# Kernel tuning notes

Hardware: AMD Instinct MI355X
Metric: run time of the kernel (lower is better)

Reference implementation:

```python
import math
import jax, jax.numpy as jnp
import numpy as np

D_MODEL, STATE_DIM, SEQ_L = 256, 64, 8192


def setup_inputs() -> dict:
    key = jax.random.key(0)
    ks = jax.random.split(key, 6)
    d, N = D_MODEL, STATE_DIM
    s = 1.0 / math.sqrt(N)
    return {
        "Lambda_re": jax.random.normal(ks[0], (d, N), jnp.float32),
        "Lambda_im": jax.random.normal(ks[1], (d, N), jnp.float32),
        "P_re": jax.random.normal(ks[2], (d, N), jnp.float32) * s,
        "P_im": jax.random.normal(ks[3], (d, N), jnp.float32) * s,
        "B_re": jax.random.normal(ks[4], (d, N), jnp.float32) * s,
        "B_im": jnp.zeros((d, N), jnp.float32),
        "log_dt": jax.random.uniform(ks[5], (d,), jnp.float32,
                                     math.log(1e-3), math.log(0.1)),
        "D": jnp.zeros((d,), jnpp := jnp.float32) if False else jnp.zeros((d,), jnp.float32),
        "L": SEQ_L,
    }


def reference(Lambda_re, Lambda_im, P_re, P_im, B_re, B_im, log_dt, D, L):
    # NPLR / Cauchy-Woodbury S4 kernel (learn_cd=False -> C = B, D is a zero buffer)
    Lam = (-jax.nn.softplus(Lambda_re) + 1j * Lambda_im).astype(jnp.complex64)  # [d, N]
    P = (P_re + 1j * P_im).astype(jnp.complex64)                                # [d, N]
    B = (B_re + 1j * B_im).astype(jnp.complex64)                                # [d, N]
    dt = jnp.exp(log_dt)                                                        # [d]

    k = jnp.arange(L)
    z = jnp.exp((-2j * jnp.pi / L) * k).astype(jnp.complex64)                   # [L] roots of unity
    eps = jnp.finfo(jnp.float32).eps
    denom_z = 1.0 + z
    denom_z = jnp.where(jnp.abs(denom_z) < eps, jnp.complex64(eps), denom_z)

    # Bilinear-transform frequencies g: [d, L] complex
    g = (2.0 / dt)[:, None] * ((1.0 - z) / denom_z)[None, :]

    # Cauchy resolvent R: [d, L, N] complex (the dominant intermediate)
    R = 1.0 / (g[:, :, None] - Lam[:, None, :])

    Pc, Bc = jnp.conj(P), jnp.conj(B)
    PRB = jnp.einsum('dn,dln,dn->dl', Pc, R, B)
    PRP = jnp.einsum('dn,dln,dn->dl', Pc, R, P)
    BRB = jnp.einsum('dn,dln,dn->dl', Bc, R, B)
    BRP = jnp.einsum('dn,dln,dn->dl', Bc, R, P)

    # Woodbury rank-1 correction, then undo the bilinear prefactor
    K_hat = (2.0 / denom_z)[None, :] * (BRB - BRP * PRB / (1.0 + PRP))          # [d, L]
    K = jnp.fft.ifft(K_hat, n=L, axis=-1).real.astype(jnp.float32)
    return (K, D)
```

## Files before the change

### kernel.cpp

```cpp
#include <hip/hip_runtime.h>
#include <math.h>

#ifndef M_PI
#define M_PI 3.14159265358979323846
#endif

#define DMODEL 256
#define NSTATE 64
#define LSEQ   8192
#define INVL   (1.0f/8192.0f)

#define OFF_TW  0
#define OFF_DN  (6144*8)
#define OFF_CDT (OFF_DN + DMODEL*NSTATE*48)

__device__ __forceinline__ float sin_rev(float r) {
#if __has_builtin(__builtin_amdgcn_sinf)
  return __builtin_amdgcn_sinf(r);
#else
  return __sinf(r * 6.283185307179586f);
#endif
}
__device__ __forceinline__ float cos_rev(float r) {
#if __has_builtin(__builtin_amdgcn_cosf)
  return __builtin_amdgcn_cosf(r);
#else
  return __cosf(r * 6.283185307179586f);
#endif
}

__device__ __forceinline__ float2 cmul(float2 a, float2 b) {
  return make_float2(a.x*b.x - a.y*b.y, a.x*b.y + a.y*b.x);
}

__device__ __forceinline__ float2 woodbury(float2 S1, float2 S2, float2 S3,
                                           float2 S4, float T) {
  float nr = (S1.x*S1.x - S1.y*S1.y) + (S2.x*S2.x - S2.y*S2.y);
  float ni = 2.0f*(S1.x*S1.y + S2.x*S2.y);
  float dr = 1.0f + S3.x, di = S3.y;
  float inv = __builtin_amdgcn_rcpf(fmaf(dr, dr, di*di));
  float qr = (nr*dr + ni*di) * inv;
  float qi = (ni*dr - nr*di) * inv;
  float vr = S4.x - qr, vi = S4.y - qi;
  return make_float2((vr - T*vi)*INVL, (vi + T*vr)*INVL);
}

__global__ __launch_bounds__(256) void precompute_kernel(
    const float* __restrict__ Lre, const float* __restrict__ Lim,
    const float* __restrict__ Pre, const float* __restrict__ Pim,
    const float* __restrict__ Bre, const float* __restrict__ Bim,
    const float* __restrict__ log_dt, char* __restrict__ ws)
{
  const int t = blockIdx.x * blockDim.x + threadIdx.x;
  float2* tw  = (float2*)(ws + OFF_TW);
  float4* dn  = (float4*)(ws + OFF_DN);
  float*  cdt = (float*)(ws + OFF_CDT);

  if (t < 6144) {
    double th = (2.0 * M_PI / (double)LSEQ) * (double)t;
    double s, c; sincos(th, &s, &c);
    tw[t] = make_float2((float)c, (float)s);
  }
  {
    float lre = Lre[t], lim = Lim[t];
    float pre = Pre[t], pim = Pim[t];
    float bre = Bre[t], bim = Bim[t];
    float sp = fmaxf(lre, 0.0f) + log1pf(expf(-fabsf(lre)));
    float w1r = pre*bre + pim*bim;
    float w1i = pre*bim - pim*bre;
    float w2  = pre*pre + pim*pim;
    float w3  = bre*bre + bim*bim;
    dn[3*t]   = make_float4(lim, sp*sp, w1r, w1i);
    dn[3*t+1] = make_float4(w2, w3, w1r*sp, w1i*sp);
    dn[3*t+2] = make_float4(w2*sp, w3*sp, 0.0f, 0.0f);
  }
  if (t < DMODEL) cdt[t] = 2.0f * expf(-log_dt[t]);
}

__global__ __launch_bounds__(1024) void fused_kernel(
    const float4* __restrict__ dn_all, const float* __restrict__ cdt,
    const float2* __restrict__ tw, const float* __restrict__ Din,
    float* __restrict__ out)
{
  __shared__ __align__(16) float2 xy[LSEQ];
  const int d = blockIdx.x;
  const int t = threadIdx.x;
  const float4* dn = dn_all + (size_t)d * (3*NSTATE);
  const float c = cdt[d];

  float TA[4], TB[4], gA[4], gB[4];
  float2 S[4][8];
#pragma unroll
  for (int j = 0; j < 4; ++j) {
    const int b = t + (j << 10);
    const unsigned p = (unsigned)(2*b);
    const unsigned r = __brev(p) >> 19;
    const int kA = (int)((r & 0x1000u) | ((r & 0x0555u) << 1) | ((r & 0x0AAAu) >> 1));
    const float rev = (float)kA * (1.0f/16384.0f);
    const float sA = sin_rev(rev), cA = cos_rev(rev);
    float ta = sA * __builtin_amdgcn_rcpf(cA);
    float tb = -cA * __builtin_amdgcn_rcpf(sA);
    ta = fminf(fmaxf(ta, -1e7f), 1e7f);
    tb = fminf(fmaxf(tb, -1e7f), 1e7f);
    TA[j] = ta; TB[j] = tb;
    gA[j] = c * ta; gB[j] = c * tb;
#pragma unroll
    for (int q = 0; q < 8; ++q) S[j][q] = make_float2(0.0f, 0.0f);
  }

#pragma unroll 4
  for (int n = 0; n < NSTATE; ++n) {
    const float4 q0 = dn[3*n];
    const float4 q1 = dn[3*n+1];
    const float4 q2 = dn[3*n+2];
#pragma unroll
    for (int j = 0; j < 4; ++j) {
      {
        const float dim = gA[j] - q0.x;
        const float inv = __builtin_amdgcn_rcpf(fmaf(dim, dim, q0.y));
        const float v = dim * inv;
        S[j][0].x = fmaf(q1.z, inv, S[j][0].x);  S[j][0].y = fmaf(-q0.z, v, S[j][0].y);
        S[j][1].x = fmaf(q1.w, inv, S[j][1].x);  S[j][1].y = fmaf(-q0.w, v, S[j][1].y);
        S[j][2].x = fmaf(q2.x, inv, S[j][2].x);  S[j][2].y = fmaf(-q1.x, v, S[j][2].y);
        S[j][3].x = fmaf(q2.y, inv, S[j][3].x);  S[j][3].y = fmaf(-q1.y, v, S[j][3].y);
      }
      {
        const float dim = gB[j] - q0.x;
        const float inv = __builtin_amdgcn_rcpf(fmaf(dim, dim, q0.y));
        const float v = dim * inv;
        S[j][4].x = fmaf(q1.z, inv, S[j][4].x);  S[j][4].y = fmaf(-q0.z, v, S[j][4].y);
        S[j][5].x = fmaf(q1.w, inv, S[j][5].x);  S[j][5].y = fmaf(-q0.w, v, S[j][5].y);
        S[j][6].x = fmaf(q2.x, inv, S[j][6].x);  S[j][6].y = fmaf(-q1.x, v, S[j][6].y);
        S[j][7].x = fmaf(q2.y, inv, S[j][7].x);  S[j][7].y = fmaf(-q1.y, v, S[j][7].y);
      }
    }
  }

#pragma unroll
  for (int j = 0; j < 4; ++j) {
    const float2 KA = woodbury(S[j][0], S[j][1], S[j][2], S[j][3], TA[j]);
    const float2 KB = woodbury(S[j][4], S[j][5], S[j][6], S[j][7], TB[j]);
    ((float4*)xy)[t + (j << 10)] = make_float4(KA.x + KB.x, KA.y + KB.y,
                                               KA.x - KB.x, KA.y - KB.y);
  }
  __syncthreads();

#pragma unroll
  for (int s = 0; s < 6; ++s) {
    const int h = 2 << (2*s);
    const int twsh = 10 - 2*s;
#pragma unroll
    for (int j = 0; j < 2; ++j) {
      const int bb = t + (j << 10);
      const int pos = bb & (h - 1);
      const int i0 = ((bb >> (1 + 2*s)) << (3 + 2*s)) + pos;
      const int ti = pos << twsh;
      const float2 w1 = tw[ti];
      const float2 w2 = tw[2*ti];
      const float2 w3 = tw[3*ti];
      const float2 x0 = xy[i0];
      const float2 x1 = xy[i0 + h];
      const float2 x2 = xy[i0 + 2*h];
      const float2 x3 = xy[i0 + 3*h];
      const float2 t1 = cmul(w1, x1);
      const float2 t2 = cmul(w2, x2);
      const float2 t3 = cmul(w3, x3);
      const float2 u0 = make_float2(x0.x + t2.x, x0.y + t2.y);
      const float2 u1 = make_float2(x0.x - t2.x, x0.y - t2.y);
      const float2 u2 = make_float2(t1.x + t3.x, t1.y + t3.y);
      const float2 vv = make_float2(t1.x - t3.x, t1.y - t3.y);
      xy[i0]         = make_float2(u0.x + u2.x, u0.y + u2.y);
      xy[i0 + h]     = make_float2(u1.x - vv.y, u1.y + vv.x);
      xy[i0 + 2*h]   = make_float2(u0.x - u2.x, u0.y - u2.y);
      xy[i0 + 3*h]   = make_float2(u1.x + vv.y, u1.y - vv.x);
    }
    __syncthreads();
  }

  float* orow = out + (size_t)d * LSEQ;
#pragma unroll
  for (int j = 0; j < 8; ++j) orow[t + (j << 10)] = xy[t + (j << 10)].x;

  if (d == 0 && t < DMODEL) out[(size_t)DMODEL * LSEQ + t] = Din[t];
}

extern "C" void kernel_launch(void* const* d_in, const int* in_sizes, int n_in,
                              void* d_out, int out_size, void* d_ws, size_t ws_size,
                              hipStream_t stream)
{
  const float* Lre    = (const float*)d_in[0];
  const float* Lim    = (const float*)d_in[1];
  const float* Pre    = (const float*)d_in[2];
  const float* Pim    = (const float*)d_in[3];
  const float* Bre    = (const float*)d_in[4];
  const float* Bim    = (const float*)d_in[5];
  const float* log_dt = (const float*)d_in[6];
  const float* Din    = (const float*)d_in[7];
  float* out = (float*)d_out;
  char* ws = (char*)d_ws;

  hipLaunchKernelGGL(precompute_kernel, dim3(64), dim3(256), 0, stream,
                     Lre, Lim, Pre, Pim, Bre, Bim, log_dt, ws);
  hipLaunchKernelGGL(fused_kernel, dim3(DMODEL), dim3(1024), 0, stream,
                     (const float4*)(ws + OFF_DN), (const float*)(ws + OFF_CDT),
                     (const float2*)(ws + OFF_TW), Din, out);
}
```

Baseline: 124.9 us.

## Vectorize Cauchy accumulation with packed FP32 ops and split into two passes

Rewrites the per-state Cauchy inner loop to use v_pk_add/mul/fma_f32 on A/B frequency pairs, with a duplicated, pre-negated parameter layout (five float4 per state) so packed operands line up. The four frequency groups per thread are processed in two passes of two to cut live accumulator registers, and launch bounds now request a minimum occupancy. This halves VALU instruction count in the hot loop but adds more global/cache loads per state and a serial outer loop.

```diff
diff --git a/kernel.cpp b/kernel.cpp
--- a/kernel.cpp
+++ b/kernel.cpp
@@ -12,7 +12,7 @@
 
 #define OFF_TW  0
 #define OFF_DN  (6144*8)
-#define OFF_CDT (OFF_DN + DMODEL*NSTATE*48)
+#define OFF_CDT (OFF_DN + DMODEL*NSTATE*80)
 
 __device__ __forceinline__ float sin_rev(float r) {
 #if __has_builtin(__builtin_amdgcn_sinf)
@@ -31,6 +31,16 @@
 
 __device__ __forceinline__ float2 cmul(float2 a, float2 b) {
   return make_float2(a.x*b.x - a.y*b.y, a.x*b.y + a.y*b.x);
+}
+
+__device__ __forceinline__ float2 pk_add(float2 a, float2 b) {
+  float2 d; asm("v_pk_add_f32 %0, %1, %2" : "=v"(d) : "v"(a), "v"(b)); return d;
+}
+__device__ __forceinline__ float2 pk_mul(float2 a, float2 b) {
+  float2 d; asm("v_pk_mul_f32 %0, %1, %2" : "=v"(d) : "v"(a), "v"(b)); return d;
+}
+__device__ __forceinline__ float2 pk_fma(float2 a, float2 b, float2 c) {
+  float2 d; asm("v_pk_fma_f32 %0, %1, %2, %3" : "=v"(d) : "v"(a), "v"(b), "v"(c)); return d;
 }
 
 __device__ __forceinline__ float2 woodbury(float2 S1, float2 S2, float2 S3,
@@ -70,14 +80,16 @@
     float w1i = pre*bim - pim*bre;
     float w2  = pre*pre + pim*pim;
     float w3  = bre*bre + bim*bim;
-    dn[3*t]   = make_float4(lim, sp*sp, w1r, w1i);
-    dn[3*t+1] = make_float4(w2, w3, w1r*sp, w1i*sp);
-    dn[3*t+2] = make_float4(w2*sp, w3*sp, 0.0f, 0.0f);
+    dn[5*t]   = make_float4(-lim, -lim, sp*sp, sp*sp);
+    dn[5*t+1] = make_float4(w1r*sp, w1r*sp, w1i*sp, w1i*sp);
+    dn[5*t+2] = make_float4(w2*sp, w2*sp, w3*sp, w3*sp);
+    dn[5*t+3] = make_float4(-w1r, -w1r, -w1i, -w1i);
+    dn[5*t+4] = make_float4(-w2, -w2, -w3, -w3);
   }
   if (t < DMODEL) cdt[t] = 2.0f * expf(-log_dt[t]);
 }
 
-__global__ __launch_bounds__(1024) void fused_kernel(
+__global__ __launch_bounds__(1024, 4) void fused_kernel(
     const float4* __restrict__ dn_all, const float* __restrict__ cdt,
     const float2* __restrict__ tw, const float* __restrict__ Din,
     float* __restrict__ out)
@@ -85,63 +97,84 @@
   __shared__ __align__(16) float2 xy[LSEQ];
   const int d = blockIdx.x;
   const int t = threadIdx.x;
-  const float4* dn = dn_all + (size_t)d * (3*NSTATE);
   const float c = cdt[d];
 
-  float TA[4], TB[4], gA[4], gB[4];
-  float2 S[4][8];
-#pragma unroll
-  for (int j = 0; j < 4; ++j) {
-    const int b = t + (j << 10);
-    const unsigned p = (unsigned)(2*b);
-    const unsigned r = __brev(p) >> 19;
-    const int kA = (int)((r & 0x1000u) | ((r & 0x0555u) << 1) | ((r & 0x0AAAu) >> 1));
-    const float rev = (float)kA * (1.0f/16384.0f);
-    const float sA = sin_rev(rev), cA = cos_rev(rev);
-    float ta = sA * __builtin_amdgcn_rcpf(cA);
-    float tb = -cA * __builtin_amdgcn_rcpf(sA);
-    ta = fminf(fmaxf(ta, -1e7f), 1e7f);
-    tb = fminf(fmaxf(tb, -1e7f), 1e7f);
-    TA[j] = ta; TB[j] = tb;
-    gA[j] = c * ta; gB[j] = c * tb;
-#pragma unroll
-    for (int q = 0; q < 8; ++q) S[j][q] = make_float2(0.0f, 0.0f);
-  }
-
-#pragma unroll 4
-  for (int n = 0; n < NSTATE; ++n) {
-    const float4 q0 = dn[3*n];
-    const float4 q1 = dn[3*n+1];
-    const float4 q2 = dn[3*n+2];
-#pragma unroll
-    for (int j = 0; j < 4; ++j) {
-      {
-        const float dim = gA[j] - q0.x;
-        const float inv = __builtin_amdgcn_rcpf(fmaf(dim, dim, q0.y));
-        const float v = dim * inv;
-        S[j][0].x = fmaf(q1.z, inv, S[j][0].x);  S[j][0].y = fmaf(-q0.z, v, S[j][0].y);
-        S[j][1].x = fmaf(q1.w, inv, S[j][1].x);  S[j][1].y = fmaf(-q0.w, v, S[j][1].y);
-        S[j][2].x = fmaf(q2.x, inv, S[j][2].x);  S[j][2].y = fmaf(-q1.x, v, S[j][2].y);
-        S[j][3].x = fmaf(q2.y, inv, S[j][3].x);  S[j][3].y = fmaf(-q1.y, v, S[j][3].y);
+  const float4* dnv = dn_all + (size_t)d * (5*NSTATE);
+  asm("" : "+v"(dnv));
+
+  for (int pass = 0; pass < 2; ++pass) {
+    float TA[2], TB[2];
+    float2 gAB[2];
+    float2 S[2][8];
+#pragma unroll
+    for (int j = 0; j < 2; ++j) {
+      const int b = t + ((2*pass + j) << 10);
+      const unsigned p = (unsigned)(2*b);
+      const unsigned r = __brev(p) >> 19;
+      const int kA = (int)((r & 0x1000u) | ((r & 0x0555u) << 1) | ((r & 0x0AAAu) >> 1));
+      const float rev = (float)kA * (1.0f/16384.0f);
+      const float sA = sin_rev(rev), cA = cos_rev(rev);
+      float ta = sA * __builtin_amdgcn_rcpf(cA);
+      float tb = -cA * __builtin_amdgcn_rcpf(sA);
+      ta = fminf(fmaxf(ta, -1e7f), 1e7f);
+      tb = fminf(fmaxf(tb, -1e7f), 1e7f);
+      TA[j] = ta; TB[j] = tb;
+      gAB[j] = make_float2(c * ta, c * tb);
+#pragma unroll
+      for (int q = 0; q < 8; ++q) S[j][q] = make_float2(0.0f, 0.0f);
+    }
+
+#pragma unroll 2
+    for (int n = 0; n < NSTATE; ++n) {
+      const float4 e0 = dnv[5*n];
+      const float4 e1 = dnv[5*n+1];
+      const float4 e2 = dnv[5*n+2];
+      const float4 e3 = dnv[5*n+3];
+      const float4 e4 = dnv[5*n+4];
+      const float2 nl2  = make_float2(e0.x, e0.y);
+      const float2 s2_2 = make_float2(e0.z, e0.w);
+      const float2 w1rs = make_float2(e1.x, e1.y);
+      const float2 w1is = make_float2(e1.z, e1.w);
+      const float2 w2s  = make_float2(e2.x, e2.y);
+      const float2 w3s  = make_float2(e2.z, e2.w);
+      const float2 nw1r = make_float2(e3.x, e3.y);
+      const float2 nw1i = make_float2(e3.z, e3.w);
+      const float2 nw2  = make_float2(e4.x, e4.y);
+      const float2 nw3  = make_float2(e4.z, e4.w);
+#pragma unroll
+      for (int j = 0; j < 2; ++j) {
+        const float2 dimAB = pk_add(gAB[j], nl2);
+        const float2 denAB = pk_fma(dimAB, dimAB, s2_2);
+        float2 invAB;
+        invAB.x = __builtin_amdgcn_rcpf(denAB.x);
+        invAB.y = __builtin_amdgcn_rcpf(denAB.y);
+        const float2 vAB = pk_mul(dimAB, invAB);
+        S[j][0] = pk_fma(w1rs, invAB, S[j][0]);
+        S[j][1] = pk_fma(w1is, invAB, S[j][1]);
+        S[j][2] = pk_fma(w2s,  invAB, S[j][2]);
+        S[j][3] = pk_fma(w3s,  invAB, S[j][3]);
+        S[j][4] = pk_fma(nw1r, vAB, S[j][4]);
+        S[j][5] = pk_fma(nw1i, vAB, S[j][5]);
+        S[j][6] = pk_fma(nw2,  vAB, S[j][6]);
+        S[j][7] = pk_fma(nw3,  vAB, S[j][7]);
       }
-      {
-        const float dim = gB[j] - q0.x;
-        const float inv = __builtin_amdgcn_rcpf(fmaf(dim, dim, q0.y));
-        const float v = dim * inv;
-        S[j][4].x = fmaf(q1.z, inv, S[j][4].x);  S[j][4].y = fmaf(-q0.z, v, S[j][4].y);
-        S[j][5].x = fmaf(q1.w, inv, S[j][5].x);  S[j][5].y = fmaf(-q0.w, v, S[j][5].y);
-        S[j][6].x = fmaf(q2.x, inv, S[j][6].x);  S[j][6].y = fmaf(-q1.x, v, S[j][6].y);
-        S[j][7].x = fmaf(q2.y, inv, S[j][7].x);  S[j][7].y = fmaf(-q1.y, v, S[j][7].y);
-      }
-    }
-  }
-
-#pragma unroll
-  for (int j = 0; j < 4; ++j) {
-    const float2 KA = woodbury(S[j][0], S[j][1], S[j][2], S[j][3], TA[j]);
-    const float2 KB = woodbury(S[j][4], S[j][5], S[j][6], S[j][7], TB[j]);
-    ((float4*)xy)[t + (j << 10)] = make_float4(KA.x + KB.x, KA.y + KB.y,
-                                               KA.x - KB.x, KA.y - KB.y);
+    }
+
+#pragma unroll
+    for (int j = 0; j < 2; ++j) {
+      const float2 S1A = make_float2(S[j][0].x, S[j][4].x);
+      const float2 S2A = make_float2(S[j][1].x, S[j][5].x);
+      const float2 S3A = make_float2(S[j][2].x, S[j][6].x);
+      const float2 S4A = make_float2(S[j][3].x, S[j][7].x);
+      const float2 S1B = make_float2(S[j][0].y, S[j][4].y);
+      const float2 S2B = make_float2(S[j][1].y, S[j][5].y);
+      const float2 S3B = make_float2(S[j][2].y, S[j][6].y);
+      const float2 S4B = make_float2(S[j][3].y, S[j][7].y);
+      const float2 KA = woodbury(S1A, S2A, S3A, S4A, TA[j]);
+      const float2 KB = woodbury(S1B, S2B, S3B, S4B, TB[j]);
+      ((float4*)xy)[t + ((2*pass + j) << 10)] =
+          make_float4(KA.x + KB.x, KA.y + KB.y, KA.x - KB.x, KA.y - KB.y);
+    }
   }
   __syncthreads();
 
```

Measured after the change: 161.6 us. +29.4%, slower.

## Split Cauchy+FFT per channel into four segment blocks plus global final radix-4 pass

Applied to the files above, without the earlier changes.

The Cauchy evaluation and the first FFT stages move into a kernel that launches four 512-thread blocks per channel, each owning a 2048-point segment in shared memory. The last radix-4 stage runs in a separate finish kernel that reads the segments from a global workspace. This replaces 256 large 1024-thread blocks with 1024 smaller ones to raise occupancy and CU coverage, and the Cauchy inner loop now keeps one frequency pair per thread, cutting register pressure. The cost is a global round trip of the full complex spectrum and an extra launch. The fused kernel is kept as a fallback when the workspace is too small.

```diff
diff --git a/kernel.cpp b/kernel.cpp
--- a/kernel.cpp
+++ b/kernel.cpp
@@ -13,6 +13,8 @@
 #define OFF_TW  0
 #define OFF_DN  (6144*8)
 #define OFF_CDT (OFF_DN + DMODEL*NSTATE*48)
+#define OFF_XY  (OFF_CDT + 1024)
+#define WS_NEED ((size_t)OFF_XY + (size_t)DMODEL*LSEQ*8)
 
 __device__ __forceinline__ float sin_rev(float r) {
 #if __has_builtin(__builtin_amdgcn_sinf)
@@ -45,6 +47,65 @@
   return make_float2((vr - T*vi)*INVL, (vi + T*vr)*INVL);
 }
 
+__device__ __forceinline__ void radix4(float2& x0, float2& x1, float2& x2, float2& x3,
+                                       float2 w1, float2 w2, float2 w3) {
+  const float2 t1 = cmul(w1, x1);
+  const float2 t2 = cmul(w2, x2);
+  const float2 t3 = cmul(w3, x3);
+  const float2 u0 = make_float2(x0.x + t2.x, x0.y + t2.y);
+  const float2 u1 = make_float2(x0.x - t2.x, x0.y - t2.y);
+  const float2 u2 = make_float2(t1.x + t3.x, t1.y + t3.y);
+  const float2 vv = make_float2(t1.x - t3.x, t1.y - t3.y);
+  x0 = make_float2(u0.x + u2.x, u0.y + u2.y);
+  x1 = make_float2(u1.x - vv.y, u1.y + vv.x);
+  x2 = make_float2(u0.x - u2.x, u0.y - u2.y);
+  x3 = make_float2(u1.x + vv.y, u1.y - vv.x);
+}
+
+__device__ __forceinline__ float4 cauchy_pair(const float4* __restrict__ dnp,
+                                              const float c, const int b) {
+  const unsigned p = (unsigned)(2*b);
+  const unsigned r = __brev(p) >> 19;
+  const int kA = (int)((r & 0x1000u) | ((r & 0x0555u) << 1) | ((r & 0x0AAAu) >> 1));
+  const float rev = (float)kA * (1.0f/16384.0f);
+  const float sA = sin_rev(rev), cA = cos_rev(rev);
+  float TA = sA * __builtin_amdgcn_rcpf(cA);
+  float TB = -cA * __builtin_amdgcn_rcpf(sA);
+  TA = fminf(fmaxf(TA, -1e7f), 1e7f);
+  TB = fminf(fmaxf(TB, -1e7f), 1e7f);
+  const float gA = c * TA, gB = c * TB;
+
+  float2 s1a={0,0}, s2a={0,0}, s3a={0,0}, s4a={0,0};
+  float2 s1b={0,0}, s2b={0,0}, s3b={0,0}, s4b={0,0};
+#pragma unroll 2
+  for (int n = 0; n < NSTATE; ++n) {
+    const float4 q0 = dnp[3*n];
+    const float4 q1 = dnp[3*n+1];
+    const float4 q2 = dnp[3*n+2];
+    {
+      const float dim = q0.x - gA;
+      const float inv = __builtin_amdgcn_rcpf(fmaf(dim, dim, q0.y));
+      const float v = dim * inv;
+      s1a.x = fmaf(q0.z, inv, s1a.x);  s1a.y = fmaf(q1.z, v, s1a.y);
+      s2a.x = fmaf(q0.w, inv, s2a.x);  s2a.y = fmaf(q1.w, v, s2a.y);
+      s3a.x = fmaf(q1.x, inv, s3a.x);  s3a.y = fmaf(q2.x, v, s3a.y);
+      s4a.x = fmaf(q1.y, inv, s4a.x);  s4a.y = fmaf(q2.y, v, s4a.y);
+    }
+    {
+      const float dim = q0.x - gB;
+      const float inv = __builtin_amdgcn_rcpf(fmaf(dim, dim, q0.y));
+      const float v = dim * inv;
+      s1b.x = fmaf(q0.z, inv, s1b.x);  s1b.y = fmaf(q1.z, v, s1b.y);
+      s2b.x = fmaf(q0.w, inv, s2b.x);  s2b.y = fmaf(q1.w, v, s2b.y);
+      s3b.x = fmaf(q1.x, inv, s3b.x);  s3b.y = fmaf(q2.x, v, s3b.y);
+      s4b.x = fmaf(q1.y, inv, s4b.x);  s4b.y = fmaf(q2.y, v, s4b.y);
+    }
+  }
+  const float2 KA = woodbury(s1a, s2a, s3a, s4a, TA);
+  const float2 KB = woodbury(s1b, s2b, s3b, s4b, TB);
+  return make_float4(KA.x + KB.x, KA.y + KB.y, KA.x - KB.x, KA.y - KB.y);
+}
+
 __global__ __launch_bounds__(256) void precompute_kernel(
     const float* __restrict__ Lre, const float* __restrict__ Lim,
     const float* __restrict__ Pre, const float* __restrict__ Pim,
@@ -70,11 +131,78 @@
     float w1i = pre*bim - pim*bre;
     float w2  = pre*pre + pim*pim;
     float w3  = bre*bre + bim*bim;
-    dn[3*t]   = make_float4(lim, sp*sp, w1r, w1i);
-    dn[3*t+1] = make_float4(w2, w3, w1r*sp, w1i*sp);
-    dn[3*t+2] = make_float4(w2*sp, w3*sp, 0.0f, 0.0f);
+    dn[3*t]   = make_float4(lim, sp*sp, w1r*sp, w1i*sp);
+    dn[3*t+1] = make_float4(w2*sp, w3*sp, w1r, w1i);
+    dn[3*t+2] = make_float4(w2, w3, 0.0f, 0.0f);
   }
   if (t < DMODEL) cdt[t] = 2.0f * expf(-log_dt[t]);
+}
+
+__global__ __launch_bounds__(512, 8) void cauchyfft_kernel(
+    const float4* __restrict__ dn_all, const float* __restrict__ cdt,
+    const float2* __restrict__ tw, float2* __restrict__ xy_ws)
+{
+  __shared__ __align__(16) float2 xy[2048];
+  const int d   = blockIdx.x >> 2;
+  const int seg = blockIdx.x & 3;
+  const int t   = threadIdx.x;
+  const float c = cdt[d];
+  const float4* dnp = dn_all + (size_t)d * (3*NSTATE);
+
+#pragma unroll
+  for (int pass = 0; pass < 2; ++pass) {
+    const int bl = t + (pass << 9);
+    ((float4*)xy)[bl] = cauchy_pair(dnp, c, (seg << 10) + bl);
+  }
+  __syncthreads();
+
+#pragma unroll
+  for (int s = 0; s < 4; ++s) {
+    const int h = 2 << (2*s);
+    const int twsh = 10 - 2*s;
+    const int pos = t & (h - 1);
+    const int i0 = ((t >> (1 + 2*s)) << (3 + 2*s)) + pos;
+    const int ti = pos << twsh;
+    float2 x0 = xy[i0], x1 = xy[i0 + h], x2 = xy[i0 + 2*h], x3 = xy[i0 + 3*h];
+    radix4(x0, x1, x2, x3, tw[ti], tw[2*ti], tw[3*ti]);
+    xy[i0] = x0; xy[i0 + h] = x1; xy[i0 + 2*h] = x2; xy[i0 + 3*h] = x3;
+    __syncthreads();
+  }
+
+  {
+    const int ti = t << 2;
+    float2 x0 = xy[t], x1 = xy[t + 512], x2 = xy[t + 1024], x3 = xy[t + 1536];
+    radix4(x0, x1, x2, x3, tw[ti], tw[2*ti], tw[3*ti]);
+    float2* xg = xy_ws + (size_t)d * LSEQ + (seg << 11);
+    xg[t] = x0; xg[t + 512] = x1; xg[t + 1024] = x2; xg[t + 1536] = x3;
+  }
+}
+
+__global__ __launch_bounds__(256) void finish_kernel(
+    const float2* __restrict__ xy_ws, const float2* __restrict__ tw,
+    const float* __restrict__ Din, float* __restrict__ out)
+{
+  const int d   = blockIdx.x >> 3;
+  const int pos = ((blockIdx.x & 7) << 8) + threadIdx.x;
+  const float2* xr = xy_ws + (size_t)d * LSEQ;
+  const float2 x0 = xr[pos];
+  const float2 x1 = xr[pos + 2048];
+  const float2 x2 = xr[pos + 4096];
+  const float2 x3 = xr[pos + 6144];
+  const float2 w1 = tw[pos], w2 = tw[2*pos], w3 = tw[3*pos];
+  const float t1x = w1.x*x1.x - w1.y*x1.y, t1y = w1.x*x1.y + w1.y*x1.x;
+  const float t2x = w2.x*x2.x - w2.y*x2.y;
+  const float t3x = w3.x*x3.x - w3.y*x3.y, t3y = w3.x*x3.y + w3.y*x3.x;
+  const float u0 = x0.x + t2x, u1 = x0.x - t2x;
+  const float u2 = t1x + t3x, vy = t1y - t3y;
+  float* orow = out + (size_t)d * LSEQ;
+  orow[pos]        = u0 + u2;
+  orow[pos + 2048] = u1 - vy;
+  orow[pos + 4096] = u0 - u2;
+  orow[pos + 6144] = u1 + vy;
+
+  if (blockIdx.x == 0) out[(size_t)DMODEL * LSEQ + threadIdx.x] =
+      (threadIdx.x < DMODEL) ? Din[threadIdx.x] : 0.0f;
 }
 
 __global__ __launch_bounds__(1024) void fused_kernel(
@@ -85,63 +213,12 @@
   __shared__ __align__(16) float2 xy[LSEQ];
   const int d = blockIdx.x;
   const int t = threadIdx.x;
-  const float4* dn = dn_all + (size_t)d * (3*NSTATE);
   const float c = cdt[d];
-
-  float TA[4], TB[4], gA[4], gB[4];
-  float2 S[4][8];
-#pragma unroll
+  const float4* dnp = dn_all + (size_t)d * (3*NSTATE);
+
   for (int j = 0; j < 4; ++j) {
     const int b = t + (j << 10);
-    const unsigned p = (unsigned)(2*b);
-    const unsigned r = __brev(p) >> 19;
-    const int kA = (int)((r & 0x1000u) | ((r & 0x0555u) << 1) | ((r & 0x0AAAu) >> 1));
-    const float rev = (float)kA * (1.0f/16384.0f);
-    const float sA = sin_rev(rev), cA = cos_rev(rev);
-    float ta = sA * __builtin_amdgcn_rcpf(cA);
-    float tb = -cA * __builtin_amdgcn_rcpf(sA);
-    ta = fminf(fmaxf(ta, -1e7f), 1e7f);
-    tb = fminf(fmaxf(tb, -1e7f), 1e7f);
-    TA[j] = ta; TB[j] = tb;
-    gA[j] = c * ta; gB[j] = c * tb;
-#pragma unroll
-    for (int q = 0; q < 8; ++q) S[j][q] = make_float2(0.0f, 0.0f);
-  }
-
-#pragma unroll 4
-  for (int n = 0; n < NSTATE; ++n) {
-    const float4 q0 = dn[3*n];
-    const float4 q1 = dn[3*n+1];
-    const float4 q2 = dn[3*n+2];
-#pragma unroll
-    for (int j = 0; j < 4; ++j) {
-      {
-        const float dim = gA[j] - q0.x;
-        const float inv = __builtin_amdgcn_rcpf(fmaf(dim, dim, q0.y));
-        const float v = dim * inv;
-        S[j][0].x = fmaf(q1.z, inv, S[j][0].x);  S[j][0].y = fmaf(-q0.z, v, S[j][0].y);
-        S[j][1].x = fmaf(q1.w, inv, S[j][1].x);  S[j][1].y = fmaf(-q0.w, v, S[j][1].y);
-        S[j][2].x = fmaf(q2.x, inv, S[j][2].x);  S[j][2].y = fmaf(-q1.x, v, S[j][2].y);
-        S[j][3].x = fmaf(q2.y, inv, S[j][3].x);  S[j][3].y = fmaf(-q1.y, v, S[j][3].y);
-      }
-      {
-        const float dim = gB[j] - q0.x;
-        const float inv = __builtin_amdgcn_rcpf(fmaf(dim, dim, q0.y));
-        const float v = dim * inv;
-        S[j][4].x = fmaf(q1.z, inv, S[j][4].x);  S[j][4].y = fmaf(-q0.z, v, S[j][4].y);
-        S[j][5].x = fmaf(q1.w, inv, S[j][5].x);  S[j][5].y = fmaf(-q0.w, v, S[j][5].y);
-        S[j][6].x = fmaf(q2.x, inv, S[j][6].x);  S[j][6].y = fmaf(-q1.x, v, S[j][6].y);
-        S[j][7].x = fmaf(q2.y, inv, S[j][7].x);  S[j][7].y = fmaf(-q1.y, v, S[j][7].y);
-      }
-    }
-  }
-
-#pragma unroll
-  for (int j = 0; j < 4; ++j) {
-    const float2 KA = woodbury(S[j][0], S[j][1], S[j][2], S[j][3], TA[j]);
-    const float2 KB = woodbury(S[j][4], S[j][5], S[j][6], S[j][7], TB[j]);
-    ((float4*)xy)[t + (j << 10)] = make_float4(KA.x + KB.x, KA.y + KB.y,
-                                               KA.x - KB.x, KA.y - KB.y);
+    ((float4*)xy)[b] = cauchy_pair(dnp, c, b);
   }
   __syncthreads();
 
@@ -155,32 +232,15 @@
       const int pos = bb & (h - 1);
       const int i0 = ((bb >> (1 + 2*s)) << (3 + 2*s)) + pos;
       const int ti = pos << twsh;
-      const float2 w1 = tw[ti];
-      const float2 w2 = tw[2*ti];
-      const float2 w3 = tw[3*ti];
-      const float2 x0 = xy[i0];
-      const float2 x1 = xy[i0 + h];
-      const float2 x2 = xy[i0 + 2*h];
-      const float2 x3 = xy[i0 + 3*h];
-      const float2 t1 = cmul(w1, x1);
-      const float2 t2 = cmul(w2, x2);
-      const float2 t3 = cmul(w3, x3);
-      const float2 u0 = make_float2(x0.x + t2.x, x0.y + t2.y);
-      const float2 u1 = make_float2(x0.x - t2.x, x0.y - t2.y);
-      const float2 u2 = make_float2(t1.x + t3.x, t1.y + t3.y);
-      const float2 vv = make_float2(t1.x - t3.x, t1.y - t3.y);
-      xy[i0]         = make_float2(u0.x + u2.x, u0.y + u2.y);
-      xy[i0 + h]     = make_float2(u1.x - vv.y, u1.y + vv.x);
-      xy[i0 + 2*h]   = make_float2(u0.x - u2.x, u0.y - u2.y);
-      xy[i0 + 3*h]   = make_float2(u1.x + vv.y, u1.y - vv.x);
+      float2 x0 = xy[i0], x1 = xy[i0 + h], x2 = xy[i0 + 2*h], x3 = xy[i0 + 3*h];
+      radix4(x0, x1, x2, x3, tw[ti], tw[2*ti], tw[3*ti]);
+      xy[i0] = x0; xy[i0 + h] = x1; xy[i0 + 2*h] = x2; xy[i0 + 3*h] = x3;
     }
     __syncthreads();
   }
 
   float* orow = out + (size_t)d * LSEQ;
-#pragma unroll
-  for (int j = 0; j < 8; ++j) orow[t + (j << 10)] = xy[t + (j << 10)].x;
-
+  for (int i = t; i < LSEQ; i += 1024) orow[i] = xy[i].x;
   if (d == 0 && t < DMODEL) out[(size_t)DMODEL * LSEQ + t] = Din[t];
 }
 
@@ -201,7 +261,17 @@
 
   hipLaunchKernelGGL(precompute_kernel, dim3(64), dim3(256), 0, stream,
                      Lre, Lim, Pre, Pim, Bre, Bim, log_dt, ws);
-  hipLaunchKernelGGL(fused_kernel, dim3(DMODEL), dim3(1024), 0, stream,
-                     (const float4*)(ws + OFF_DN), (const float*)(ws + OFF_CDT),
-                     (const float2*)(ws + OFF_TW), Din, out);
-}
+
+  if (ws_size >= WS_NEED) {
+    hipLaunchKernelGGL(cauchyfft_kernel, dim3(DMODEL * 4), dim3(512), 0, stream,
+                       (const float4*)(ws + OFF_DN), (const float*)(ws + OFF_CDT),
+                       (const float2*)(ws + OFF_TW), (float2*)(ws + OFF_XY));
+    hipLaunchKernelGGL(finish_kernel, dim3(DMODEL * 8), dim3(256), 0, stream,
+                       (const float2*)(ws + OFF_XY), (const float2*)(ws + OFF_TW),
+                       Din, out);
+  } else {
+    hipLaunchKernelGGL(fused_kernel, dim3(DMODEL), dim3(1024), 0, stream,
+                       (const float4*)(ws + OFF_DN), (const float*)(ws + OFF_CDT),
+                       (const float2*)(ws + OFF_TW), Din, out);
+  }
+}
```

After: 128.0 us. 2.5% more time.
